# Performance work log

Measured on AMD Instinct MI355X. Metric: run time of the kernel, lower is better.

The kernel has to match this reference:

```python
import jax, jax.numpy as jnp
import numpy as np

B, D, L = 8, 512, 8192


def log_g(x):
    # th.where(x >= 0, log(relu(x) + 1), x)
    return jnp.where(x >= 0, jnp.log1p(jnp.maximum(x, 0.0)), x)


def min_gru(hg):
    # hg: [B, H, L] -> [B, H/2, L]
    h, gate = jnp.split(hg, 2, axis=1)
    log_coeffs = -jax.nn.softplus(gate)                      # log a_t
    log_values = -jax.nn.softplus(-gate) + log_g(h)          # log b_t
    a_star = jnp.cumsum(log_coeffs, axis=2)
    log_h0_plus_b_star = jax.lax.cumlogsumexp(log_values - a_star, axis=2)
    return jnp.exp(a_star + log_h0_plus_b_star)


def conv1x1(x, w, b):
    # x: [B, D, L], w: [E, D], b: [E]  (kernel-size-1 Conv1d == pointwise linear)
    return jnp.einsum('ed,bdl->bel', w, x) + b[None, :, None]


def setup_inputs() -> dict:
    key = jax.random.key(0)
    k1, k2, k3, k4, k5 = jax.random.split(key, 5)
    scale = 1.0 / np.sqrt(D)
    x = jax.random.normal(k1, (B, D, L), dtype=jnp.float32)
    w_fore = jax.random.normal(k2, (D, D), dtype=jnp.float32) * scale
    b_fore = jax.random.normal(k3, (D,), dtype=jnp.float32) * scale
    w_back = jax.random.normal(k4, (D, D), dtype=jnp.float32) * scale
    b_back = jax.random.normal(k5, (D,), dtype=jnp.float32) * scale
    return {'x': x, 'w_fore': w_fore, 'b_fore': b_fore, 'w_back': w_back, 'b_back': b_back}


def reference(x, w_fore, b_fore, w_back, b_back):
    fore = min_gru(conv1x1(x, w_fore, b_fore))                            # [B, D/2, L]
    back = jnp.flip(min_gru(conv1x1(jnp.flip(x, 2), w_back, b_back)), 2)  # [B, D/2, L]
    return jnp.concatenate([fore, back], axis=1)                          # [B, D, L]
```

## Files before the change

### kernel.cpp

```cpp
#include <hip/hip_runtime.h>

#define BATCH 8
#define DIN   512
#define SEQ   8192
#define ECH   1024
#define HCH   256
#define CL    32
#define NCHNK (SEQ / CL)
#define NSC   16

typedef __bf16 bf16;
typedef __bf16 bf16x8 __attribute__((ext_vector_type(8)));
typedef __bf16 bf16x4 __attribute__((ext_vector_type(4)));
typedef float  floatx4 __attribute__((ext_vector_type(4)));

__device__ __forceinline__ void async_ld16(void* lds, const void* g) {
  __builtin_amdgcn_global_load_lds(
      (const __attribute__((address_space(1))) unsigned int*)g,
      (__attribute__((address_space(3))) unsigned int*)lds, 16, 0, 0);
}

__device__ __forceinline__ float bits2f(unsigned u) {
  return __builtin_bit_cast(float, u);
}

__device__ __forceinline__ void gru_ab(unsigned v, float& a, float& bt) {
  float hh = bits2f(v << 16);
  float g  = bits2f(v & 0xffff0000u);
  float eg = __expf(-g);
  float sg = 1.f / (1.f + eg);
  a = eg * sg;
  float gv = hh >= 0.f ? 1.f + hh : __expf(hh);
  bt = sg * gv;
}

__global__ void k_wconv(const float* __restrict__ wf, const float* __restrict__ bfo,
                        const float* __restrict__ wb, const float* __restrict__ bb,
                        bf16* __restrict__ Wb, float* __restrict__ bias) {
  int idx = blockIdx.x * 256 + threadIdx.x;
  if (idx < ECH * DIN) {
    int n = idx >> 9, d = idx & 511;
    int dir = n >> 9, r = n & 511, e = r >> 1, isg = r & 1;
    int s = e + (isg ? HCH : 0);
    const float* w = dir ? wb : wf;
    Wb[idx] = (bf16)w[s * DIN + d];
  }
  if (idx < ECH) {
    int dir = idx >> 9, r = idx & 511, e = r >> 1, isg = r & 1;
    int s = e + (isg ? HCH : 0);
    bias[idx] = (dir ? bb : bfo)[s];
  }
}

__global__ void k_xpose(const float* __restrict__ x, bf16* __restrict__ xT) {
  __shared__ float T[64 * 65];
  int t = threadIdx.x;
  int l0 = blockIdx.x * 64;
  int d0 = blockIdx.y * 64;
  int b  = blockIdx.z;
  const float* xb = x + (size_t)b * DIN * SEQ;
#pragma unroll
  for (int p = 0; p < 4; ++p) {
    int dl = (t >> 4) + p * 16;
    int l4 = (t & 15) * 4;
    float4 v = *(const float4*)(xb + (size_t)(d0 + dl) * SEQ + l0 + l4);
    T[dl * 65 + l4 + 0] = v.x;
    T[dl * 65 + l4 + 1] = v.y;
    T[dl * 65 + l4 + 2] = v.z;
    T[dl * 65 + l4 + 3] = v.w;
  }
  __syncthreads();
  bf16* xTb = xT + (size_t)b * SEQ * DIN;
#pragma unroll
  for (int p = 0; p < 2; ++p) {
    int ll = (t >> 3) + p * 32;
    int d8 = (t & 7) * 8;
    bf16x8 h;
#pragma unroll
    for (int j = 0; j < 8; ++j) h[j] = (bf16)T[(d8 + j) * 65 + ll];
    *(bf16x8*)(xTb + (size_t)(l0 + ll) * DIN + d0 + d8) = h;
  }
}

__launch_bounds__(256, 4)
__global__ void k_gemm(const bf16* __restrict__ xT, const bf16* __restrict__ Wb,
                       const float* __restrict__ bias, bf16* __restrict__ hg,
                       float* __restrict__ Asum, float* __restrict__ Bsum) {
  __shared__ bf16 lds[16896];
  bf16* As = lds;
  bf16* Bs = lds + 8192;

  int t = threadIdx.x;
  int lane = t & 63, wave = t >> 6;

  int lin = blockIdx.x + 8 * blockIdx.y;
  int xcd = lin & 7;
  int seq = lin >> 3;
  int ltile = xcd + 8 * (seq >> 3);
  int ntile = seq & 7;
  int n0 = ntile * 128;
  int l0 = ltile * 128;
  int b  = blockIdx.z;

  int l15 = lane & 15, quad = lane >> 4;
  int wm = wave >> 1, wn = wave & 1;
  int mb = wm * 64, nb = wn * 64;

  const bf16* gA = xT + ((size_t)b * SEQ + l0) * DIN;
  const bf16* gB = Wb + (size_t)n0 * DIN;

  int srow = wave * 32 + (lane >> 3);
  int scol = (((lane & 7) ^ (lane >> 3)) * 8);

  floatx4 acc[4][4];
#pragma unroll
  for (int i = 0; i < 4; ++i)
#pragma unroll
    for (int j = 0; j < 4; ++j) acc[i][j] = (floatx4){0.f, 0.f, 0.f, 0.f};

  for (int kt = 0; kt < DIN / 64; ++kt) {
    int k0 = kt * 64;
#pragma unroll
    for (int q = 0; q < 4; ++q) {
      async_ld16(As + (wave * 32 + q * 8) * 64,
                 gA + (size_t)(srow + q * 8) * DIN + k0 + scol);
      async_ld16(Bs + (wave * 32 + q * 8) * 64,
                 gB + (size_t)(srow + q * 8) * DIN + k0 + scol);
    }
    __syncthreads();
#pragma unroll
    for (int kk = 0; kk < 64; kk += 32) {
      int rsw = l15 & 7;
      bf16x8 af[4], bfr[4];
#pragma unroll
      for (int i = 0; i < 4; ++i)
        af[i] = *(const bf16x8*)(As + (mb + i * 16 + l15) * 64 +
                                 (((kk >> 3) + quad) ^ rsw) * 8);
#pragma unroll
      for (int i = 0; i < 4; ++i)
        bfr[i] = *(const bf16x8*)(Bs + (nb + i * 16 + l15) * 64 +
                                  (((kk >> 3) + quad) ^ rsw) * 8);
#pragma unroll
      for (int mi = 0; mi < 4; ++mi)
#pragma unroll
        for (int ni = 0; ni < 4; ++ni)
          acc[mi][ni] = __builtin_amdgcn_mfma_f32_16x16x32_bf16(
              af[mi], bfr[ni], acc[mi][ni], 0, 0, 0);
    }
    __syncthreads();
  }

  float bb4[4];
#pragma unroll
  for (int ni = 0; ni < 4; ++ni) bb4[ni] = bias[n0 + nb + ni * 16 + l15];
  bf16* Cs = lds;
#pragma unroll
  for (int mi = 0; mi < 4; ++mi)
#pragma unroll
    for (int ni = 0; ni < 4; ++ni)
#pragma unroll
      for (int r = 0; r < 4; ++r) {
        int row = mb + mi * 16 + quad * 4 + r;
        int col = nb + ni * 16 + l15;
        Cs[row * 132 + col] = (bf16)(acc[mi][ni][r] + bb4[ni]);
      }
  __syncthreads();
  bf16* hgb = hg + ((size_t)b * SEQ + l0) * ECH + n0;
#pragma unroll
  for (int p = 0; p < 8; ++p) {
    int row = p * 16 + (t >> 4);
    int seg = t & 15;
    *(bf16x8*)(hgb + (size_t)row * ECH + seg * 8) =
        *(const bf16x8*)(Cs + row * 132 + seg * 8);
  }

  {
    int dirn = ntile >> 2;
    int c = wave, el = lane;
    float A = 1.f, Bc = 0.f;
#pragma unroll 8
    for (int i = 0; i < CL; ++i) {
      int row = c * CL + (dirn ? (CL - 1 - i) : i);
      unsigned v = *(const unsigned*)(Cs + row * 132 + 2 * el);
      float a, bt;
      gru_ab(v, a, bt);
      A *= a;
      Bc = a * Bc + bt;
    }
    int chunkg = ltile * 4 + c;
    int eg = ((n0 & 511) >> 1) + el;
    size_t o = ((size_t)(b * 2 + dirn) * NCHNK + chunkg) * 256 + eg;
    Asum[o] = A;
    Bsum[o] = Bc;
  }
}

__global__ void k_scan2a(const float* __restrict__ Asum, const float* __restrict__ Bsum,
                         float* __restrict__ SA, float* __restrict__ SB) {
  int e = threadIdx.x, sc = blockIdx.x, row2 = blockIdx.y, dir = row2 & 1;
  size_t base = (size_t)row2 * NCHNK;
  float Acc = 1.f, Bcc = 0.f;
#pragma unroll
  for (int i = 0; i < 16; ++i) {
    int c = sc * 16 + (dir ? 15 - i : i);
    size_t o = (base + c) * 256 + e;
    float a = Asum[o], bv = Bsum[o];
    Acc = a * Acc;
    Bcc = a * Bcc + bv;
  }
  size_t so = ((size_t)row2 * NSC + sc) * 256 + e;
  SA[so] = Acc;
  SB[so] = Bcc;
}

__global__ void k_scan2b(const float* __restrict__ SA, const float* __restrict__ SB,
                         float* __restrict__ hsc) {
  int e = threadIdx.x, row2 = blockIdx.x, dir = row2 & 1;
  float h = 0.f;
  for (int i = 0; i < NSC; ++i) {
    int sc = dir ? NSC - 1 - i : i;
    size_t o = ((size_t)row2 * NSC + sc) * 256 + e;
    hsc[o] = h;
    h = SA[o] * h + SB[o];
  }
}

__global__ void k_scan2c(const float* __restrict__ Asum, const float* __restrict__ Bsum,
                         const float* __restrict__ hsc, float* __restrict__ hin) {
  int e = threadIdx.x, sc = blockIdx.x, row2 = blockIdx.y, dir = row2 & 1;
  float h = hsc[((size_t)row2 * NSC + sc) * 256 + e];
#pragma unroll
  for (int i = 0; i < 16; ++i) {
    int c = sc * 16 + (dir ? 15 - i : i);
    size_t o = ((size_t)row2 * NCHNK + c) * 256 + e;
    hin[o] = h;
    h = Asum[o] * h + Bsum[o];
  }
}

__global__ void k_scan3(const bf16* __restrict__ hg, const float* __restrict__ hin,
                        float* __restrict__ out) {
  __shared__ float T[512 * 33];
  int t = threadIdx.x;
  int chunk = blockIdx.x, b = blockIdx.y;
  int dir = t >> 8;
  int p = t & 255;
  const bf16* hb = hg + (size_t)b * SEQ * ECH + dir * 512 + 2 * p;
  float h = hin[((size_t)(b * 2 + dir) * NCHNK + chunk) * 256 + p];
  int lbase = chunk * CL;
#pragma unroll 8
  for (int i = 0; i < CL; ++i) {
    int ll = dir ? (CL - 1 - i) : i;
    unsigned v = *(const unsigned*)(hb + (size_t)(lbase + ll) * ECH);
    float a, bt;
    gru_ab(v, a, bt);
    h = a * h + bt;
    T[t * 33 + ll] = h;
  }
  __syncthreads();
  float* ob = out + (size_t)b * 512 * SEQ + lbase;
#pragma unroll
  for (int q = 0; q < 8; ++q) {
    int row = q * 64 + (t >> 3);
    int c4 = (t & 7) * 4;
    float4 v4;
    v4.x = T[row * 33 + c4 + 0];
    v4.y = T[row * 33 + c4 + 1];
    v4.z = T[row * 33 + c4 + 2];
    v4.w = T[row * 33 + c4 + 3];
    *(float4*)(ob + (size_t)row * SEQ + c4) = v4;
  }
}

extern "C" void kernel_launch(void* const* d_in, const int* in_sizes, int n_in,
                              void* d_out, int out_size, void* d_ws, size_t ws_size,
                              hipStream_t stream) {
  const float* x   = (const float*)d_in[0];
  const float* wf  = (const float*)d_in[1];
  const float* bfo = (const float*)d_in[2];
  const float* wb  = (const float*)d_in[3];
  const float* bb  = (const float*)d_in[4];
  float* out = (float*)d_out;
  char* ws = (char*)d_ws;

  bf16*  xT   = (bf16*)(ws);
  bf16*  hg   = (bf16*)(ws + 67108864);
  bf16*  Wbm  = (bf16*)(ws + 201326592);
  float* bias = (float*)(ws + 202375168);
  float* Asum = (float*)(ws + 202379264);
  float* Bsum = (float*)(ws + 206573568);
  float* hin  = (float*)(ws + 210767872);
  float* SA   = (float*)(ws + 214962176);
  float* SB   = (float*)(ws + 215224320);
  float* hsc  = (float*)(ws + 215486464);

  k_wconv<<<2048, 256, 0, stream>>>(wf, bfo, wb, bb, Wbm, bias);
  k_xpose<<<dim3(SEQ / 64, DIN / 64, BATCH), 256, 0, stream>>>(x, xT);
  k_gemm<<<dim3(ECH / 128, SEQ / 128, BATCH), 256, 0, stream>>>(xT, Wbm, bias, hg,
                                                                Asum, Bsum);
  k_scan2a<<<dim3(NSC, 16), 256, 0, stream>>>(Asum, Bsum, SA, SB);
  k_scan2b<<<16, 256, 0, stream>>>(SA, SB, hsc);
  k_scan2c<<<dim3(NSC, 16), 256, 0, stream>>>(Asum, Bsum, hsc, hin);
  k_scan3<<<dim3(NCHNK, BATCH), 512, 0, stream>>>(hg, hin, out);
}
```

Before: 420.7 us.

## Use 32x32x16 MFMA with pre-swizzled register-loaded weights; single-pass chunk scan

The GEMM moves from 16x16x32 to 32x32x16 bf16 MFMA tiles. The weight matrix is pre-packed into a fragment-ready layout so each lane loads its B operand straight from global memory into registers, skipping LDS staging for B and halving the shared-memory traffic per k-step. The three-kernel hierarchical scan over chunk summaries is replaced by one sequential 256-step scan kernel, which removes two launches but serialises the carry across chunks on only 16 blocks. Loading weights directly from global adds latency that is not hidden by double buffering.

```diff
diff --git a/kernel.cpp b/kernel.cpp
--- a/kernel.cpp
+++ b/kernel.cpp
@@ -7,12 +7,12 @@
 #define HCH   256
 #define CL    32
 #define NCHNK (SEQ / CL)
-#define NSC   16
 
 typedef __bf16 bf16;
 typedef __bf16 bf16x8 __attribute__((ext_vector_type(8)));
 typedef __bf16 bf16x4 __attribute__((ext_vector_type(4)));
-typedef float  floatx4 __attribute__((ext_vector_type(4)));
+typedef float  floatx4  __attribute__((ext_vector_type(4)));
+typedef float  floatx16 __attribute__((ext_vector_type(16)));
 
 __device__ __forceinline__ void async_ld16(void* lds, const void* g) {
   __builtin_amdgcn_global_load_lds(
@@ -36,14 +36,19 @@
 
 __global__ void k_wconv(const float* __restrict__ wf, const float* __restrict__ bfo,
                         const float* __restrict__ wb, const float* __restrict__ bb,
-                        bf16* __restrict__ Wb, float* __restrict__ bias) {
+                        bf16* __restrict__ Wf, float* __restrict__ bias) {
   int idx = blockIdx.x * 256 + threadIdx.x;
   if (idx < ECH * DIN) {
-    int n = idx >> 9, d = idx & 511;
+    int j    = idx & 7;
+    int lane = (idx >> 3) & 63;
+    int g    = (idx >> 9) & 31;
+    int n5   = idx >> 14;
+    int n = n5 * 32 + (lane & 31);
+    int k = g * 16 + (lane >> 5) * 8 + j;
     int dir = n >> 9, r = n & 511, e = r >> 1, isg = r & 1;
     int s = e + (isg ? HCH : 0);
     const float* w = dir ? wb : wf;
-    Wb[idx] = (bf16)w[s * DIN + d];
+    Wf[idx] = (bf16)w[s * DIN + k];
   }
   if (idx < ECH) {
     int dir = idx >> 9, r = idx & 511, e = r >> 1, isg = r & 1;
@@ -83,12 +88,11 @@
 }
 
 __launch_bounds__(256, 4)
-__global__ void k_gemm(const bf16* __restrict__ xT, const bf16* __restrict__ Wb,
+__global__ void k_gemm(const bf16* __restrict__ xT, const bf16* __restrict__ Wf,
                        const float* __restrict__ bias, bf16* __restrict__ hg,
                        float* __restrict__ Asum, float* __restrict__ Bsum) {
   __shared__ bf16 lds[16896];
   bf16* As = lds;
-  bf16* Bs = lds + 8192;
 
   int t = threadIdx.x;
   int lane = t & 63, wave = t >> 6;
@@ -102,67 +106,65 @@
   int l0 = ltile * 128;
   int b  = blockIdx.z;
 
-  int l15 = lane & 15, quad = lane >> 4;
+  int l31 = lane & 31, half = lane >> 5;
   int wm = wave >> 1, wn = wave & 1;
   int mb = wm * 64, nb = wn * 64;
 
-  const bf16* gA = xT + ((size_t)b * SEQ + l0) * DIN;
-  const bf16* gB = Wb + (size_t)n0 * DIN;
+  const bf16* gA  = xT + ((size_t)b * SEQ + l0) * DIN;
+  const bf16* gBf = Wf + (size_t)((n0 + nb) >> 5) * 16384 + lane * 8;
 
   int srow = wave * 32 + (lane >> 3);
   int scol = (((lane & 7) ^ (lane >> 3)) * 8);
 
-  floatx4 acc[4][4];
-#pragma unroll
-  for (int i = 0; i < 4; ++i)
-#pragma unroll
-    for (int j = 0; j < 4; ++j) acc[i][j] = (floatx4){0.f, 0.f, 0.f, 0.f};
+  floatx16 acc[2][2];
+#pragma unroll
+  for (int i = 0; i < 2; ++i)
+#pragma unroll
+    for (int j = 0; j < 2; ++j)
+#pragma unroll
+      for (int r = 0; r < 16; ++r) acc[i][j][r] = 0.f;
 
   for (int kt = 0; kt < DIN / 64; ++kt) {
     int k0 = kt * 64;
 #pragma unroll
-    for (int q = 0; q < 4; ++q) {
+    for (int q = 0; q < 4; ++q)
       async_ld16(As + (wave * 32 + q * 8) * 64,
                  gA + (size_t)(srow + q * 8) * DIN + k0 + scol);
-      async_ld16(Bs + (wave * 32 + q * 8) * 64,
-                 gB + (size_t)(srow + q * 8) * DIN + k0 + scol);
+    bf16x8 bf8[2][4];
+#pragma unroll
+    for (int ni = 0; ni < 2; ++ni)
+#pragma unroll
+      for (int ks = 0; ks < 4; ++ks)
+        bf8[ni][ks] = *(const bf16x8*)(gBf + ni * 16384 + (kt * 4 + ks) * 512);
+    __syncthreads();
+#pragma unroll
+    for (int ks = 0; ks < 4; ++ks) {
+#pragma unroll
+      for (int mi = 0; mi < 2; ++mi) {
+        bf16x8 af = *(const bf16x8*)(As + (mb + mi * 32 + l31) * 64 +
+                                     (((ks * 2 + half) ^ (lane & 7)) * 8));
+        acc[mi][0] = __builtin_amdgcn_mfma_f32_32x32x16_bf16(af, bf8[0][ks],
+                                                             acc[mi][0], 0, 0, 0);
+        acc[mi][1] = __builtin_amdgcn_mfma_f32_32x32x16_bf16(af, bf8[1][ks],
+                                                             acc[mi][1], 0, 0, 0);
+      }
     }
     __syncthreads();
-#pragma unroll
-    for (int kk = 0; kk < 64; kk += 32) {
-      int rsw = l15 & 7;
-      bf16x8 af[4], bfr[4];
-#pragma unroll
-      for (int i = 0; i < 4; ++i)
-        af[i] = *(const bf16x8*)(As + (mb + i * 16 + l15) * 64 +
-                                 (((kk >> 3) + quad) ^ rsw) * 8);
-#pragma unroll
-      for (int i = 0; i < 4; ++i)
-        bfr[i] = *(const bf16x8*)(Bs + (nb + i * 16 + l15) * 64 +
-                                  (((kk >> 3) + quad) ^ rsw) * 8);
-#pragma unroll
-      for (int mi = 0; mi < 4; ++mi)
-#pragma unroll
-        for (int ni = 0; ni < 4; ++ni)
-          acc[mi][ni] = __builtin_amdgcn_mfma_f32_16x16x32_bf16(
-              af[mi], bfr[ni], acc[mi][ni], 0, 0, 0);
-    }
-    __syncthreads();
-  }
-
-  float bb4[4];
-#pragma unroll
-  for (int ni = 0; ni < 4; ++ni) bb4[ni] = bias[n0 + nb + ni * 16 + l15];
+  }
+
+  float bb2[2];
+#pragma unroll
+  for (int ni = 0; ni < 2; ++ni) bb2[ni] = bias[n0 + nb + ni * 32 + l31];
   bf16* Cs = lds;
 #pragma unroll
-  for (int mi = 0; mi < 4; ++mi)
-#pragma unroll
-    for (int ni = 0; ni < 4; ++ni)
-#pragma unroll
-      for (int r = 0; r < 4; ++r) {
-        int row = mb + mi * 16 + quad * 4 + r;
-        int col = nb + ni * 16 + l15;
-        Cs[row * 132 + col] = (bf16)(acc[mi][ni][r] + bb4[ni]);
+  for (int mi = 0; mi < 2; ++mi)
+#pragma unroll
+    for (int ni = 0; ni < 2; ++ni)
+#pragma unroll
+      for (int r = 0; r < 16; ++r) {
+        int row = mb + mi * 32 + 4 * half + (r & 3) + 8 * (r >> 2);
+        int col = nb + ni * 32 + l31;
+        Cs[row * 132 + col] = (bf16)(acc[mi][ni][r] + bb2[ni]);
       }
   __syncthreads();
   bf16* hgb = hg + ((size_t)b * SEQ + l0) * ECH + n0;
@@ -195,44 +197,15 @@
   }
 }
 
-__global__ void k_scan2a(const float* __restrict__ Asum, const float* __restrict__ Bsum,
-                         float* __restrict__ SA, float* __restrict__ SB) {
-  int e = threadIdx.x, sc = blockIdx.x, row2 = blockIdx.y, dir = row2 & 1;
+__global__ void k_scan2(const float* __restrict__ Asum, const float* __restrict__ Bsum,
+                        float* __restrict__ hin) {
+  int e = threadIdx.x, row2 = blockIdx.x, dir = row2 & 1;
   size_t base = (size_t)row2 * NCHNK;
-  float Acc = 1.f, Bcc = 0.f;
-#pragma unroll
-  for (int i = 0; i < 16; ++i) {
-    int c = sc * 16 + (dir ? 15 - i : i);
+  float h = 0.f;
+#pragma unroll 8
+  for (int i = 0; i < NCHNK; ++i) {
+    int c = dir ? (NCHNK - 1 - i) : i;
     size_t o = (base + c) * 256 + e;
-    float a = Asum[o], bv = Bsum[o];
-    Acc = a * Acc;
-    Bcc = a * Bcc + bv;
-  }
-  size_t so = ((size_t)row2 * NSC + sc) * 256 + e;
-  SA[so] = Acc;
-  SB[so] = Bcc;
-}
-
-__global__ void k_scan2b(const float* __restrict__ SA, const float* __restrict__ SB,
-                         float* __restrict__ hsc) {
-  int e = threadIdx.x, row2 = blockIdx.x, dir = row2 & 1;
-  float h = 0.f;
-  for (int i = 0; i < NSC; ++i) {
-    int sc = dir ? NSC - 1 - i : i;
-    size_t o = ((size_t)row2 * NSC + sc) * 256 + e;
-    hsc[o] = h;
-    h = SA[o] * h + SB[o];
-  }
-}
-
-__global__ void k_scan2c(const float* __restrict__ Asum, const float* __restrict__ Bsum,
-                         const float* __restrict__ hsc, float* __restrict__ hin) {
-  int e = threadIdx.x, sc = blockIdx.x, row2 = blockIdx.y, dir = row2 & 1;
-  float h = hsc[((size_t)row2 * NSC + sc) * 256 + e];
-#pragma unroll
-  for (int i = 0; i < 16; ++i) {
-    int c = sc * 16 + (dir ? 15 - i : i);
-    size_t o = ((size_t)row2 * NCHNK + c) * 256 + e;
     hin[o] = h;
     h = Asum[o] * h + Bsum[o];
   }
@@ -285,21 +258,16 @@
 
   bf16*  xT   = (bf16*)(ws);
   bf16*  hg   = (bf16*)(ws + 67108864);
-  bf16*  Wbm  = (bf16*)(ws + 201326592);
+  bf16*  Wfm  = (bf16*)(ws + 201326592);
   float* bias = (float*)(ws + 202375168);
   float* Asum = (float*)(ws + 202379264);
   float* Bsum = (float*)(ws + 206573568);
   float* hin  = (float*)(ws + 210767872);
-  float* SA   = (float*)(ws + 214962176);
-  float* SB   = (float*)(ws + 215224320);
-  float* hsc  = (float*)(ws + 215486464);
-
-  k_wconv<<<2048, 256, 0, stream>>>(wf, bfo, wb, bb, Wbm, bias);
+
+  k_wconv<<<2048, 256, 0, stream>>>(wf, bfo, wb, bb, Wfm, bias);
   k_xpose<<<dim3(SEQ / 64, DIN / 64, BATCH), 256, 0, stream>>>(x, xT);
-  k_gemm<<<dim3(ECH / 128, SEQ / 128, BATCH), 256, 0, stream>>>(xT, Wbm, bias, hg,
+  k_gemm<<<dim3(ECH / 128, SEQ / 128, BATCH), 256, 0, stream>>>(xT, Wfm, bias, hg,
                                                                 Asum, Bsum);
-  k_scan2a<<<dim3(NSC, 16), 256, 0, stream>>>(Asum, Bsum, SA, SB);
-  k_scan2b<<<16, 256, 0, stream>>>(SA, SB, hsc);
-  k_scan2c<<<dim3(NSC, 16), 256, 0, stream>>>(Asum, Bsum, hsc, hin);
+  k_scan2<<<16, 256, 0, stream>>>(Asum, Bsum, hin);
   k_scan3<<<dim3(NCHNK, BATCH), 512, 0, stream>>>(hg, hin, out);
 }
```

Result: slower. 429.4 us (+2.1%).
